# Performance work log

Measured on AMD Instinct MI355X. Metric: run time of the kernel, lower is better.

## Reference

```python
import jax, jax.numpy as jnp
import numpy as np

B, T, I, H, L = 128, 512, 64, 512, 64  # batch, seq_len, input=latent size, hidden
DEC_STEPS = 100  # hardcoded in the original decoder loop


def _lstm_cell(x, h, c, Wih, Whh, bih, bhh):
    # PyTorch gate order: i, f, g, o
    gates = x @ Wih.T + h @ Whh.T + bih + bhh  # [B, 4H]
    i, f, g, o = jnp.split(gates, 4, axis=-1)
    c = jax.nn.sigmoid(f) * c + jax.nn.sigmoid(i) * jnp.tanh(g)
    h = jax.nn.sigmoid(o) * jnp.tanh(c)
    return h, c


def setup_inputs() -> dict:
    key = jax.random.key(0)
    ks = jax.random.split(key, 18)
    u = lambda k, shape, fan: jax.random.uniform(k, shape, jnp.float32, -1.0, 1.0) / np.sqrt(fan).astype(np.float32)
    return {
        "sequences": jax.random.normal(ks[0], (B, T, I), jnp.float32),
        "seq_lengths": jnp.full((B,), T, dtype=jnp.int32),
        "eps": jax.random.normal(ks[1], (B, L), jnp.float32),
        "W_ih_enc": u(ks[2], (4 * H, I), H), "W_hh_enc": u(ks[3], (4 * H, H), H),
        "b_ih_enc": u(ks[4], (4 * H,), H), "b_hh_enc": u(ks[5], (4 * H,), H),
        "W_mean": u(ks[6], (L, H), H), "b_mean": u(ks[7], (L,), H),
        "W_logvar": u(ks[8], (L, H), H), "b_logvar": u(ks[9], (L,), H),
        "W_init": u(ks[10], (H, L), L), "b_init": u(ks[11], (H,), L),
        "W_ih_dec": u(ks[12], (4 * H, I), H), "W_hh_dec": u(ks[13], (4 * H, H), H),
        "b_ih_dec": u(ks[14], (4 * H,), H), "b_hh_dec": u(ks[15], (4 * H,), H),
        "W_out": u(ks[16], (I, H), H), "b_out": u(ks[17], (I,), H),
    }


def _forward(sequences, eps,
             W_ih_enc, W_hh_enc, b_ih_enc, b_hh_enc,
             W_mean, b_mean, W_logvar, b_logvar,
             W_init, b_init,
             W_ih_dec, W_hh_dec, b_ih_dec, b_hh_dec,
             W_out, b_out):
    Bn = sequences.shape[0]
    h0 = jnp.zeros((Bn, H), sequences.dtype)

    # ---- encoder: full-sequence LSTM, keep only final hidden state ----
    def enc_step(carry, x_t):
        h, c = carry
        h, c = _lstm_cell(x_t, h, c, W_ih_enc, W_hh_enc, b_ih_enc, b_hh_enc)
        return (h, c), None

    (h_n, _), _ = jax.lax.scan(enc_step, (h0, h0), sequences.transpose(1, 0, 2))

    # ---- VAE reparameterization ----
    mean = h_n @ W_mean.T + b_mean
    log_var = h_n @ W_logvar.T + b_logvar
    z = mean + eps * jnp.exp(0.5 * log_var)

    h_dec = z @ W_init.T + b_init
    c_dec = jnp.zeros_like(h_dec)
    x0 = jnp.zeros((Bn, L), z.dtype)

    def dec_step(carry, _):
        h, c, x = carry
        h, c = _lstm_cell(x, h, c, W_ih_dec, W_hh_dec, b_ih_dec, b_hh_dec)
        x_hat = h @ W_out.T + b_out
        return (h, c, x_hat), x_hat

    _, xs = jax.lax.scan(dec_step, (h_dec, c_dec, x0), None, length=DEC_STEPS)
    x_hat = xs.transpose(1, 0, 2)  # [B, 100, I]
    return x_hat, mean, log_var


def reference(sequences, seq_lengths, eps,
              W_ih_enc, W_hh_enc, b_ih_enc, b_hh_enc,
              W_mean, b_mean, W_logvar, b_logvar,
              W_init, b_init,
              W_ih_dec, W_hh_dec, b_ih_dec, b_hh_dec,
              W_out, b_out):
    del seq_lengths  # accepted but unused by the original forward
    return _forward(sequences, eps,
                    W_ih_enc, W_hh_enc, b_ih_enc, b_hh_enc,
                    W_mean, b_mean, W_logvar, b_logvar,
                    W_init, b_init,
                    W_ih_dec, W_hh_dec, b_ih_dec, b_hh_dec,
                    W_out, b_out)
```

## Files before the change

kernel.cpp:

```cpp
#include <hip/hip_runtime.h>
#include <stdint.h>


typedef short short8 __attribute__((ext_vector_type(8)));
typedef float f32x4 __attribute__((ext_vector_type(4)));
typedef unsigned int u32x4 __attribute__((ext_vector_type(4)));

#define WS_FLAGS  0
#define WS_HBUF0  16384
#define WS_HBUF1  147456
#define WS_Z      278528
#define WS_BCOMB  311296
#define WS_WCOMB  319488
#define WS_SEQB   2416640
#define WS_END    10805248
#define WS_ZERO   WS_HBUF1

static __device__ __forceinline__ float b2f(unsigned short u) {
    return __builtin_bit_cast(float, (unsigned int)u << 16);
}
static __device__ __forceinline__ unsigned short f2b(float f) {
    unsigned int u = __builtin_bit_cast(unsigned int, f);
    unsigned int r = u + 0x7FFFu + ((u >> 16) & 1u);
    return (unsigned short)(r >> 16);
}
static __device__ __forceinline__ float sigm(float x)  { return 1.0f / (1.0f + __expf(-x)); }
static __device__ __forceinline__ float tanhx(float x) { return 1.0f - 2.0f / (__expf(2.0f * x) + 1.0f); }

static __device__ __forceinline__ short8 cvt8(const float* p) {
    const float4 a = ((const float4*)p)[0];
    const float4 b = ((const float4*)p)[1];
    short8 r;
    r[0] = (short)f2b(a.x); r[1] = (short)f2b(a.y);
    r[2] = (short)f2b(a.z); r[3] = (short)f2b(a.w);
    r[4] = (short)f2b(b.x); r[5] = (short)f2b(b.y);
    r[6] = (short)f2b(b.z); r[7] = (short)f2b(b.w);
    return r;
}

static __device__ __forceinline__ void load2x16_cc(const void* p0, const void* p1,
                                                   u32x4& v0, u32x4& v1) {
    asm volatile("global_load_dwordx4 %0, %2, off sc0 sc1\n\t"
                 "global_load_dwordx4 %1, %3, off sc0 sc1\n\t"
                 "s_waitcnt vmcnt(0)"
                 : "=&v"(v0), "=&v"(v1) : "v"(p0), "v"(p1) : "memory");
}
static __device__ __forceinline__ void store16_cc(void* p, u32x4 v) {
    asm volatile("global_store_dwordx4 %0, %1, off sc0 sc1"
                 :: "v"(p), "v"(v) : "memory");
}
static __device__ __forceinline__ void drain_vm() {
    asm volatile("s_waitcnt vmcnt(0)" ::: "memory");
}

__global__ void __launch_bounds__(256)
seqcvt_kernel(const float* __restrict__ src, unsigned short* __restrict__ dst)
{
    int i = (blockIdx.x * 256 + threadIdx.x) * 4;
    float4 v = *(const float4*)(src + i);
    uint32_t lo = (uint32_t)f2b(v.x) | ((uint32_t)f2b(v.y) << 16);
    uint32_t hi = (uint32_t)f2b(v.z) | ((uint32_t)f2b(v.w) << 16);
    uint2 o; o.x = lo; o.y = hi;
    *(uint2*)(dst + i) = o;
}

__global__ void __launch_bounds__(256)
wcomb_kernel(const float* __restrict__ Wih_d,
             const float* __restrict__ Whh_d,
             const float* __restrict__ Wout,
             const float* __restrict__ bih_d,
             const float* __restrict__ bhh_d,
             const float* __restrict__ bout,
             unsigned char* __restrict__ ws)
{
    __shared__ float Ash[64][64];
    __shared__ float Bsh[64][65];
    const int bid = blockIdx.x, t = threadIdx.x;
    const int gt0 = (bid >> 3) * 64, ht0 = (bid & 7) * 64;
    for (int j = 0; j < 16; ++j) {
        int idx = t + j * 256;
        int r = idx >> 6, c = idx & 63;
        Ash[r][c] = Wih_d[(size_t)(gt0 + r) * 64 + c];
        Bsh[r][c] = Wout[(size_t)r * 512 + ht0 + c];
    }
    __syncthreads();
    const int gl = t >> 2, hl0 = (t & 3) * 16;
    for (int hh = 0; hh < 16; ++hh) {
        float acc = 0.f;
        #pragma unroll
        for (int i = 0; i < 64; ++i) acc += Ash[gl][i] * Bsh[i][hl0 + hh];
        int g = gt0 + gl, h = ht0 + hl0 + hh;
        float v = Whh_d[(size_t)g * 512 + h] + acc;
        ((unsigned short*)(ws + WS_WCOMB))[(size_t)g * 512 + h] = f2b(v);
    }
    if ((bid & 7) == 0 && t < 64) {
        int g = gt0 + t;
        float acc = bih_d[g] + bhh_d[g];
        #pragma unroll
        for (int i = 0; i < 64; ++i) acc += bout[i] * Ash[t][i];
        ((float*)(ws + WS_BCOMB))[g] = acc;
    }
}

__global__ void __launch_bounds__(512, 2)
vae_persistent(const float* __restrict__ seq,
               const unsigned short* __restrict__ seqb,
               const float* __restrict__ eps,
               const float* __restrict__ Wih_e,
               const float* __restrict__ Whh_e,
               const float* __restrict__ bih_e,
               const float* __restrict__ bhh_e,
               const float* __restrict__ Wmean,
               const float* __restrict__ bmean,
               const float* __restrict__ Wlv,
               const float* __restrict__ blv,
               const float* __restrict__ Winit,
               const float* __restrict__ binit,
               const float* __restrict__ Whh_d,
               const float* __restrict__ bih_d,
               const float* __restrict__ bhh_d,
               const float* __restrict__ Wout,
               const float* __restrict__ bout,
               unsigned char* __restrict__ ws,
               float* __restrict__ out)
{
    __shared__ __align__(16) short Al[16 * 520];
    __shared__ __align__(16) short Ho[512];
    __shared__ float fbuf[128];
    __shared__ float zl[16 * 64];

    const int tid  = threadIdx.x;
    const int g    = blockIdx.x & 7;
    const int s    = blockIdx.x >> 3;
    const int b0   = g * 16;
    const int lane = tid & 63;
    const int wv   = tid >> 6;
    const int col  = lane & 15;
    const int q    = lane >> 4;
    const int nloc = wv * 16 + col;
    const int gt   = nloc & 3;
    const int grow = gt * 512 + s * 32 + (nloc >> 2);

    uint32_t* flags = (uint32_t*)(ws + WS_FLAGS) + (size_t)g * 512;
    unsigned char* hbuf0 = ws + WS_HBUF0;
    unsigned char* hbuf1 = ws + WS_HBUF1;
    uint32_t* zbuf = (uint32_t*)(ws + WS_Z);

    float cst[4] = {0.f, 0.f, 0.f, 0.f};

    auto wait_and_stage = [&](uint32_t R) {
        if (wv == 0 && lane < 16) {
            while (__hip_atomic_load(&flags[lane * 32], __ATOMIC_RELAXED,
                                     __HIP_MEMORY_SCOPE_AGENT) < R) {}
        }
        __syncthreads();
        const unsigned char* src = (R & 1) ? hbuf1 : hbuf0;
        const int b = tid >> 5, c = tid & 31;
        const unsigned char* p0 = src + (size_t)(b0 + b) * 1024 + c * 32;
        u32x4 v0, v1;
        load2x16_cc(p0, p0 + 16, v0, v1);
        u32x4* dst = (u32x4*)Al;
        dst[b * 65 + c * 2 + 0] = v0;
        dst[b * 65 + c * 2 + 1] = v1;
        __syncthreads();
    };

    auto publish_h = [&](uint32_t R) {
        if (wv == 0) {
            unsigned char* dst = (R & 1) ? hbuf1 : hbuf0;
            int row = lane >> 2, part = lane & 3;
            u32x4 v = ((const u32x4*)Ho)[lane];
            store16_cc(dst + (size_t)(b0 + row) * 1024 + s * 64 + part * 16, v);
            drain_vm();
            if (lane == 0)
                __hip_atomic_store(&flags[s * 32], R, __ATOMIC_RELAXED,
                                   __HIP_MEMORY_SCOPE_AGENT);
        }
    };

    short8 wfrag[16];
    auto load_wfrag_f32 = [&](const float* Wsrc) {
        #pragma unroll
        for (int kt = 0; kt < 16; ++kt)
            wfrag[kt] = cvt8(Wsrc + (size_t)grow * 512 + kt * 32 + q * 8);
    };
    auto load_wfrag_bf16 = [&](const unsigned short* Wsrc) {
        #pragma unroll
        for (int kt = 0; kt < 16; ++kt)
            wfrag[kt] = *(const short8*)((const short*)Wsrc +
                         (size_t)grow * 512 + kt * 32 + q * 8);
    };

    auto cell_update = [&](f32x4 acc) {
        float act[4];
        #pragma unroll
        for (int r = 0; r < 4; ++r)
            act[r] = (gt == 2) ? tanhx(acc[r]) : sigm(acc[r]);
        int base = lane & ~3;
        #pragma unroll
        for (int r = 0; r < 4; ++r) {
            float vi = __shfl(act[r], base + 0);
            float vf = __shfl(act[r], base + 1);
            float vg = __shfl(act[r], base + 2);
            float vo = __shfl(act[r], base + 3);
            cst[r] = vf * cst[r] + vi * vg;
            act[r] = vo * tanhx(cst[r]);
        }
        if (gt == 0) {
            int hd4 = wv * 4 + (col >> 2);
            #pragma unroll
            for (int r = 0; r < 4; ++r)
                Ho[(q * 4 + r) * 32 + hd4] = (short)f2b(act[r]);
        }
    };

    load_wfrag_f32(Whh_e);
    short8 xwf[2];
    #pragma unroll
    for (int kt = 0; kt < 2; ++kt)
        xwf[kt] = cvt8(Wih_e + (size_t)grow * 64 + kt * 32 + q * 8);
    const float bias_e = bih_e[grow] + bhh_e[grow];

    auto load_x = [&](int t, short8* xf) {
        if (seqb) {
            const short* xs = (const short*)seqb + ((size_t)(b0 + col) * 512 + t) * 64 + q * 8;
            xf[0] = *(const short8*)(xs);
            xf[1] = *(const short8*)(xs + 32);
        } else {
            const float* xs = seq + ((size_t)(b0 + col) * 512 + t) * 64 + q * 8;
            xf[0] = cvt8(xs);
            xf[1] = cvt8(xs + 32);
        }
    };

    short8 xf[2];
    load_x(0, xf);
    for (uint32_t t = 0; t < 512; ++t) {
        wait_and_stage(t);
        f32x4 acc = {bias_e, bias_e, bias_e, bias_e};
        acc = __builtin_amdgcn_mfma_f32_16x16x32_bf16(xf[0], xwf[0], acc, 0, 0, 0);
        acc = __builtin_amdgcn_mfma_f32_16x16x32_bf16(xf[1], xwf[1], acc, 0, 0, 0);
        if (t < 511) load_x(t + 1, xf);
        #pragma unroll
        for (int kt = 0; kt < 16; ++kt) {
            short8 a = *(const short8*)(Al + col * 520 + kt * 32 + q * 8);
            acc = __builtin_amdgcn_mfma_f32_16x16x32_bf16(a, wfrag[kt], acc, 0, 0, 0);
        }
        cell_update(acc);
        __syncthreads();
        publish_h(t + 1);
    }

    wait_and_stage(512);
    if (tid < 128) {
        int which = tid >> 6, idx = tid & 63;
        int b = idx >> 2, ldl = idx & 3;
        int ld = s * 4 + ldl;
        const float* wrow = (which ? Wlv : Wmean) + (size_t)ld * 512;
        float a = (which ? blv[ld] : bmean[ld]);
        for (int k = 0; k < 512; ++k)
            a += b2f((unsigned short)Al[b * 520 + k]) * wrow[k];
        out[819200 + which * 8192 + (size_t)(b0 + b) * 64 + ld] = a;
        fbuf[which * 64 + idx] = a;
    }
    __syncthreads();
    if (wv == 0) {
        int b = lane >> 2, ldl = lane & 3;
        int ld = s * 4 + ldl;
        float m = fbuf[lane], lv = fbuf[64 + lane];
        float e = eps[(size_t)(b0 + b) * 64 + ld];
        float z = m + e * __expf(0.5f * lv);
        __hip_atomic_store(zbuf + (size_t)(b0 + b) * 64 + ld,
                           __builtin_bit_cast(uint32_t, z),
                           __ATOMIC_RELAXED, __HIP_MEMORY_SCOPE_AGENT);
        drain_vm();
        if (lane == 0)
            __hip_atomic_store(&flags[s * 32], 513u,
                               __ATOMIC_RELAXED, __HIP_MEMORY_SCOPE_AGENT);
    }
    if (wv == 0 && lane < 16)
        while (__hip_atomic_load(&flags[lane * 32], __ATOMIC_RELAXED,
                                 __HIP_MEMORY_SCOPE_AGENT) < 513u) {}
    __syncthreads();

    #pragma unroll
    for (int j = 0; j < 2; ++j) {
        int idx = tid + j * 512;
        int b = idx >> 6, l = idx & 63;
        uint32_t v = __hip_atomic_load(zbuf + (size_t)(b0 + b) * 64 + l,
                                       __ATOMIC_RELAXED, __HIP_MEMORY_SCOPE_AGENT);
        zl[b * 64 + l] = __builtin_bit_cast(float, v);
    }
    __syncthreads();
    {
        int b = tid >> 5, c = tid & 31;
        #pragma unroll
        for (int j = 0; j < 16; ++j) {
            int hd = c * 16 + j;
            float a = binit[hd];
            const float* wr = Winit + (size_t)hd * 64;
            #pragma unroll
            for (int l = 0; l < 64; ++l) a += zl[b * 64 + l] * wr[l];
            Al[b * 520 + hd] = (short)f2b(a);
        }
    }
    #pragma unroll
    for (int r = 0; r < 4; ++r) cst[r] = 0.f;
    __syncthreads();

    short8 wof[16];
    float xbias = 0.f;
    if (s < 4 && wv == 7) {
        xbias = bout[s * 16 + col];
        #pragma unroll
        for (int kt = 0; kt < 16; ++kt)
            wof[kt] = cvt8(Wout + (size_t)(s * 16 + col) * 512 + kt * 32 + q * 8);
    }
    auto xhat_emit = [&](int d) {
        f32x4 a2 = {xbias, xbias, xbias, xbias};
        #pragma unroll
        for (int kt = 0; kt < 16; ++kt) {
            short8 a = *(const short8*)(Al + col * 520 + kt * 32 + q * 8);
            a2 = __builtin_amdgcn_mfma_f32_16x16x32_bf16(a, wof[kt], a2, 0, 0, 0);
        }
        #pragma unroll
        for (int r = 0; r < 4; ++r) {
            int b = q * 4 + r;
            out[((size_t)(b0 + b) * 100 + d) * 64 + s * 16 + col] = a2[r];
        }
    };

    load_wfrag_f32(Whh_d);
    float bias = bih_d[grow] + bhh_d[grow];
    for (uint32_t d = 0; d < 100; ++d) {
        if (d > 0) wait_and_stage(513 + d);
        f32x4 acc = {bias, bias, bias, bias};
        #pragma unroll
        for (int kt = 0; kt < 16; ++kt) {
            short8 a = *(const short8*)(Al + col * 520 + kt * 32 + q * 8);
            acc = __builtin_amdgcn_mfma_f32_16x16x32_bf16(a, wfrag[kt], acc, 0, 0, 0);
        }
        cell_update(acc);
        __syncthreads();
        publish_h(514 + d);
        if (d >= 1 && s < 4 && wv == 7) xhat_emit(d - 1);
        if (d == 0) {
            load_wfrag_bf16((const unsigned short*)(ws + WS_WCOMB));
            bias = ((const float*)(ws + WS_BCOMB))[grow];
        }
    }
    wait_and_stage(613);
    if (s < 4 && wv == 7) xhat_emit(99);
}

extern "C" void kernel_launch(void* const* d_in, const int* in_sizes, int n_in,
                              void* d_out, int out_size, void* d_ws, size_t ws_size,
                              hipStream_t stream) {
    (void)in_sizes; (void)n_in; (void)out_size;
    const float* seq   = (const float*)d_in[0];
    const float* eps   = (const float*)d_in[2];
    const float* Wih_e = (const float*)d_in[3];
    const float* Whh_e = (const float*)d_in[4];
    const float* bih_e = (const float*)d_in[5];
    const float* bhh_e = (const float*)d_in[6];
    const float* Wmean = (const float*)d_in[7];
    const float* bmean = (const float*)d_in[8];
    const float* Wlv   = (const float*)d_in[9];
    const float* blv   = (const float*)d_in[10];
    const float* Winit = (const float*)d_in[11];
    const float* binit = (const float*)d_in[12];
    const float* Wih_d = (const float*)d_in[13];
    const float* Whh_d = (const float*)d_in[14];
    const float* bih_d = (const float*)d_in[15];
    const float* bhh_d = (const float*)d_in[16];
    const float* Wout  = (const float*)d_in[17];
    const float* bout  = (const float*)d_in[18];
    unsigned char* ws = (unsigned char*)d_ws;
    float* out = (float*)d_out;

    const bool have_seqb = ws_size >= (size_t)WS_END;
    unsigned short* seqb = have_seqb ? (unsigned short*)(ws + WS_SEQB) : nullptr;

    hipMemsetAsync(ws, 0, WS_ZERO, stream);
    if (have_seqb)
        seqcvt_kernel<<<4096, 256, 0, stream>>>(seq, seqb);
    wcomb_kernel<<<256, 256, 0, stream>>>(Wih_d, Whh_d, Wout, bih_d, bhh_d, bout, ws);
    vae_persistent<<<128, 512, 0, stream>>>(
        seq, seqb, eps, Wih_e, Whh_e, bih_e, bhh_e,
        Wmean, bmean, Wlv, blv, Winit, binit,
        Whh_d, bih_d, bhh_d, Wout, bout, ws, out);
}
```

Measured before the change: 1.880 ms.

## Replace flag-based step barrier with parity tags embedded in hidden-state data

Removes the per-step flag handshake (drain of stores, then a flag store by the producer, and a flag poll plus barrier by the consumer). Instead, each bf16 hidden value carries a step-parity bit in its lowest mantissa bit, and consumers spin directly on the staged data until every element shows the expected tag. The aim is to take a full global round-trip and a barrier off the serial recurrence of 612 steps. In exchange, one mantissa bit of h is lost, and hbuf1 must be pre-filled with a tag pattern through an extra memset.

```diff
diff --git a/kernel.cpp b/kernel.cpp
--- a/kernel.cpp
+++ b/kernel.cpp
@@ -14,7 +14,6 @@
 #define WS_WCOMB  319488
 #define WS_SEQB   2416640
 #define WS_END    10805248
-#define WS_ZERO   WS_HBUF1
 
 static __device__ __forceinline__ float b2f(unsigned short u) {
     return __builtin_bit_cast(float, (unsigned int)u << 16);
@@ -148,17 +147,21 @@
 
     float cst[4] = {0.f, 0.f, 0.f, 0.f};
 
-    auto wait_and_stage = [&](uint32_t R) {
-        if (wv == 0 && lane < 16) {
-            while (__hip_atomic_load(&flags[lane * 32], __ATOMIC_RELAXED,
-                                     __HIP_MEMORY_SCOPE_AGENT) < R) {}
-        }
-        __syncthreads();
+    auto stage_h = [&](uint32_t R) {
         const unsigned char* src = (R & 1) ? hbuf1 : hbuf0;
+        const uint32_t want32 = ((R >> 1) & 1) ? 0x00010001u : 0u;
         const int b = tid >> 5, c = tid & 31;
         const unsigned char* p0 = src + (size_t)(b0 + b) * 1024 + c * 32;
         u32x4 v0, v1;
-        load2x16_cc(p0, p0 + 16, v0, v1);
+        for (;;) {
+            load2x16_cc(p0, p0 + 16, v0, v1);
+            uint32_t bad = ((v0[0] ^ want32) | (v0[1] ^ want32) |
+                            (v0[2] ^ want32) | (v0[3] ^ want32) |
+                            (v1[0] ^ want32) | (v1[1] ^ want32) |
+                            (v1[2] ^ want32) | (v1[3] ^ want32)) & 0x00010001u;
+            if (!bad) break;
+        }
+        __syncthreads();
         u32x4* dst = (u32x4*)Al;
         dst[b * 65 + c * 2 + 0] = v0;
         dst[b * 65 + c * 2 + 1] = v1;
@@ -168,13 +171,12 @@
     auto publish_h = [&](uint32_t R) {
         if (wv == 0) {
             unsigned char* dst = (R & 1) ? hbuf1 : hbuf0;
+            const uint32_t tag32 = ((R >> 1) & 1) ? 0x00010001u : 0u;
             int row = lane >> 2, part = lane & 3;
             u32x4 v = ((const u32x4*)Ho)[lane];
+            #pragma unroll
+            for (int i = 0; i < 4; ++i) v[i] = (v[i] & 0xFFFEFFFEu) | tag32;
             store16_cc(dst + (size_t)(b0 + row) * 1024 + s * 64 + part * 16, v);
-            drain_vm();
-            if (lane == 0)
-                __hip_atomic_store(&flags[s * 32], R, __ATOMIC_RELAXED,
-                                   __HIP_MEMORY_SCOPE_AGENT);
         }
     };
 
@@ -236,7 +238,7 @@
     short8 xf[2];
     load_x(0, xf);
     for (uint32_t t = 0; t < 512; ++t) {
-        wait_and_stage(t);
+        stage_h(t);
         f32x4 acc = {bias_e, bias_e, bias_e, bias_e};
         acc = __builtin_amdgcn_mfma_f32_16x16x32_bf16(xf[0], xwf[0], acc, 0, 0, 0);
         acc = __builtin_amdgcn_mfma_f32_16x16x32_bf16(xf[1], xwf[1], acc, 0, 0, 0);
@@ -251,7 +253,7 @@
         publish_h(t + 1);
     }
 
-    wait_and_stage(512);
+    stage_h(512);
     if (tid < 128) {
         int which = tid >> 6, idx = tid & 63;
         int b = idx >> 2, ldl = idx & 3;
@@ -275,12 +277,12 @@
                            __ATOMIC_RELAXED, __HIP_MEMORY_SCOPE_AGENT);
         drain_vm();
         if (lane == 0)
-            __hip_atomic_store(&flags[s * 32], 513u,
+            __hip_atomic_store(&flags[s * 32], 1u,
                                __ATOMIC_RELAXED, __HIP_MEMORY_SCOPE_AGENT);
     }
     if (wv == 0 && lane < 16)
         while (__hip_atomic_load(&flags[lane * 32], __ATOMIC_RELAXED,
-                                 __HIP_MEMORY_SCOPE_AGENT) < 513u) {}
+                                 __HIP_MEMORY_SCOPE_AGENT) < 1u) {}
     __syncthreads();
 
     #pragma unroll
@@ -333,7 +335,7 @@
     load_wfrag_f32(Whh_d);
     float bias = bih_d[grow] + bhh_d[grow];
     for (uint32_t d = 0; d < 100; ++d) {
-        if (d > 0) wait_and_stage(513 + d);
+        if (d > 0) stage_h(512 + d);
         f32x4 acc = {bias, bias, bias, bias};
         #pragma unroll
         for (int kt = 0; kt < 16; ++kt) {
@@ -342,14 +344,14 @@
         }
         cell_update(acc);
         __syncthreads();
-        publish_h(514 + d);
+        publish_h(513 + d);
         if (d >= 1 && s < 4 && wv == 7) xhat_emit(d - 1);
         if (d == 0) {
             load_wfrag_bf16((const unsigned short*)(ws + WS_WCOMB));
             bias = ((const float*)(ws + WS_BCOMB))[grow];
         }
     }
-    wait_and_stage(613);
+    stage_h(612);
     if (s < 4 && wv == 7) xhat_emit(99);
 }
 
@@ -381,7 +383,8 @@
     const bool have_seqb = ws_size >= (size_t)WS_END;
     unsigned short* seqb = have_seqb ? (unsigned short*)(ws + WS_SEQB) : nullptr;
 
-    hipMemsetAsync(ws, 0, WS_ZERO, stream);
+    hipMemsetAsync(ws, 0, WS_HBUF1, stream);
+    hipMemsetAsync(ws + WS_HBUF1, 0x01, WS_Z - WS_HBUF1, stream);
     if (have_seqb)
         seqcvt_kernel<<<4096, 256, 0, stream>>>(seq, seqb);
     wcomb_kernel<<<256, 256, 0, stream>>>(Wih_d, Whh_d, Wout, bih_d, bhh_d, bout, ws);
```

After: 2.459 ms. 30.8% more time.
